# Kernel optimization log

Hardware: AMD Instinct MI355X
Metric: run time of the kernel (lower is better)

The kernel has to match this reference:

```python
import jax, jax.numpy as jnp
import numpy as np

D_MODEL = 256; N_HEADS = 8; N_LEVELS = 4; N_POINTS = 4; D_FFN = 1024
BS = 8; NQ = 100; NKPT = 17
LEVEL_SHAPES = [(160, 160), (80, 80), (40, 40), (20, 20)]  # (H, W) per level
LEN_V = sum(h * w for h, w in LEVEL_SHAPES)  # 34000


def layer_norm(x, g, b, eps=1e-5):
    m = x.mean(-1, keepdims=True)
    v = ((x - m) ** 2).mean(-1, keepdims=True)
    return (x - m) * jax.lax.rsqrt(v + eps) * g + b


def mha(q, k, v, Wqkv, bqkv, Wo, bo):
    # torch nn.MultiheadAttention, batch_first, eval mode (no dropout)
    d = q.shape[-1]; dh = d // N_HEADS
    def proj(x, W, b):
        return (x @ W.T + b).reshape(*x.shape[:-1], N_HEADS, dh)
    qp = proj(q, Wqkv[:d], bqkv[:d])
    kp = proj(k, Wqkv[d:2 * d], bqkv[d:2 * d])
    vp = proj(v, Wqkv[2 * d:], bqkv[2 * d:])
    att = jnp.einsum('bqhd,bkhd->bhqk', qp, kp) / jnp.sqrt(jnp.asarray(dh, q.dtype))
    att = jax.nn.softmax(att, -1)
    out = jnp.einsum('bhqk,bkhd->bqhd', att, vp).reshape(q.shape)
    return out @ Wo.T + bo


def bilinear_sample(val, loc, h, w):
    # val: (B, H, h*w, Dh); loc: (B, Lq, H, P, 2) normalized to [0,1]
    # matches F.grid_sample(align_corners=False, padding_mode='zeros') on grid 2*loc-1
    B, Lq, H, P, _ = loc.shape
    px = loc[..., 0] * w - 0.5
    py = loc[..., 1] * h - 0.5
    x0f = jnp.floor(px); y0f = jnp.floor(py)
    lx = px - x0f; ly = py - y0f
    x0 = x0f.astype(jnp.int32); y0 = y0f.astype(jnp.int32)
    out = jnp.zeros((B, H, Lq, P, val.shape[-1]), val.dtype)
    for dx, dy, wt in ((0, 0, (1 - lx) * (1 - ly)), (1, 0, lx * (1 - ly)),
                       (0, 1, (1 - lx) * ly), (1, 1, lx * ly)):
        xi = x0 + dx; yi = y0 + dy
        valid = ((xi >= 0) & (xi < w) & (yi >= 0) & (yi < h)).astype(val.dtype)
        idx = jnp.clip(yi, 0, h - 1) * w + jnp.clip(xi, 0, w - 1)  # (B,Lq,H,P)
        idx = idx.transpose(0, 2, 1, 3).reshape(B, H, Lq * P)
        g = jnp.take_along_axis(val, idx[..., None], axis=2).reshape(B, H, Lq, P, -1)
        out = out + g * (wt * valid).transpose(0, 2, 1, 3)[..., None]
    return out  # (B, H, Lq, P, Dh)


def ms_deform_attn(query, ref_points, memory, off_W, off_b, aw_W, aw_b,
                   val_W, val_b, outp_W, outp_b):
    B, Lq, _ = query.shape
    dh = D_MODEL // N_HEADS
    value = (memory @ val_W.T + val_b).reshape(B, LEN_V, N_HEADS, dh)
    off = (query @ off_W.T + off_b).reshape(B, Lq, N_HEADS, N_LEVELS, N_POINTS, 2)
    aw = (query @ aw_W.T + aw_b).reshape(B, Lq, N_HEADS, N_LEVELS * N_POINTS)
    aw = jax.nn.softmax(aw, -1).reshape(B, Lq, N_HEADS, N_LEVELS, N_POINTS)
    normalizer = jnp.array([[w, h] for h, w in LEVEL_SHAPES], dtype=query.dtype)  # (L,2) as (W,H)
    loc = ref_points[:, :, None, :, None, :] + off / normalizer[None, None, None, :, None, :]
    out = jnp.zeros((B, Lq, N_HEADS, dh), query.dtype)
    start = 0
    for l, (h, w) in enumerate(LEVEL_SHAPES):
        vl = value[:, start:start + h * w].transpose(0, 2, 1, 3)  # (B,H,hw,Dh)
        s = bilinear_sample(vl, loc[:, :, :, l], h, w)            # (B,H,Lq,P,Dh)
        out = out + jnp.einsum('bhqpd,bqhp->bqhd', s, aw[:, :, :, l])
        start += h * w
    return out.reshape(B, Lq, D_MODEL) @ outp_W.T + outp_b


def setup_inputs() -> dict:
    key = jax.random.key(0)
    ks = iter(jax.random.split(key, 40))
    d = D_MODEL
    def w(shape, s=0.02):
        return jax.random.normal(next(ks), shape, jnp.float32) * s
    inp = {
        'tgt_pose': jax.random.normal(next(ks), (BS, NQ, NKPT, d), jnp.float32),
        'tgt_pose_query_pos': jax.random.normal(next(ks), (BS, NQ, NKPT, d), jnp.float32),
        'tgt_pose_reference_points': jax.random.uniform(next(ks), (BS, NQ * NKPT, N_LEVELS, 2), jnp.float32),
        'memory': jax.random.normal(next(ks), (BS, LEN_V, d), jnp.float32),
        'win_Wqkv': w((3 * d, d)), 'win_bqkv': jnp.zeros((3 * d,), jnp.float32),
        'win_Wo': w((d, d)), 'win_bo': jnp.zeros((d,), jnp.float32),
        'win_ng': jnp.ones((d,), jnp.float32), 'win_nb': jnp.zeros((d,), jnp.float32),
        'acr_Wqkv': w((3 * d, d)), 'acr_bqkv': jnp.zeros((3 * d,), jnp.float32),
        'acr_Wo': w((d, d)), 'acr_bo': jnp.zeros((d,), jnp.float32),
        'acr_ng': jnp.ones((d,), jnp.float32), 'acr_nb': jnp.zeros((d,), jnp.float32),
        'off_W': w((N_HEADS * N_LEVELS * N_POINTS * 2, d)),
        'off_b': jax.random.uniform(next(ks), (N_HEADS * N_LEVELS * N_POINTS * 2,), jnp.float32, -1.0, 1.0),
        'aw_W': w((N_HEADS * N_LEVELS * N_POINTS, d)), 'aw_b': jnp.zeros((N_HEADS * N_LEVELS * N_POINTS,), jnp.float32),
        'val_W': w((d, d)), 'val_b': jnp.zeros((d,), jnp.float32),
        'outp_W': w((d, d)), 'outp_b': jnp.zeros((d,), jnp.float32),
        'gate_W': w((2 * d, 2 * d)), 'gate_b': jnp.zeros((2 * d,), jnp.float32),
        'gate_ng': jnp.ones((d,), jnp.float32), 'gate_nb': jnp.zeros((d,), jnp.float32),
        'ffn_W1': w((D_FFN, d)), 'ffn_b1': jnp.zeros((D_FFN,), jnp.float32),
        'ffn_W2': w((d, D_FFN)), 'ffn_b2': jnp.zeros((d,), jnp.float32),
        'n2_g': jnp.ones((d,), jnp.float32), 'n2_b': jnp.zeros((d,), jnp.float32),
        'memory_spatial_shapes': jnp.array(LEVEL_SHAPES, jnp.int32),
    }
    return inp


def reference(tgt_pose, tgt_pose_query_pos, tgt_pose_reference_points, memory,
              win_Wqkv, win_bqkv, win_Wo, win_bo, win_ng, win_nb,
              acr_Wqkv, acr_bqkv, acr_Wo, acr_bo, acr_ng, acr_nb,
              off_W, off_b, aw_W, aw_b, val_W, val_b, outp_W, outp_b,
              gate_W, gate_b, gate_ng, gate_nb,
              ffn_W1, ffn_b1, ffn_W2, ffn_b2, n2_g, n2_b,
              memory_spatial_shapes):
    bs, nq, K, d = tgt_pose.shape
    # with_pos_embed mutates tgt_pose in place in the torch code -> residual includes pos
    tgt = tgt_pose + tgt_pose_query_pos
    # within-attention over keypoints of each query
    x = tgt.reshape(bs * nq, K, d)
    t2 = mha(x, x, x, win_Wqkv, win_bqkv, win_Wo, win_bo).reshape(bs, nq, K, d)
    tgt = layer_norm(tgt + t2, win_ng, win_nb)
    # across-attention over queries for each keypoint
    xk = tgt.transpose(0, 2, 1, 3).reshape(bs * K, nq, d)
    t2 = mha(xk, xk, xk, acr_Wqkv, acr_bqkv, acr_Wo, acr_bo)
    tgt = layer_norm(xk + t2, acr_ng, acr_nb).reshape(bs, K, nq, d).transpose(0, 2, 1, 3)
    # second in-place pos add before deformable cross-attn (also feeds gateway)
    tgt_q = tgt + tgt_pose_query_pos
    t2 = ms_deform_attn(tgt_q.reshape(bs, nq * K, d), tgt_pose_reference_points, memory,
                        off_W, off_b, aw_W, aw_b, val_W, val_b, outp_W, outp_b)
    t2 = t2.reshape(bs, nq, K, d)
    # Gate
    g = jax.nn.sigmoid(jnp.concatenate([tgt_q, t2], -1) @ gate_W.T + gate_b)
    g1, g2 = jnp.split(g, 2, -1)
    tgt = layer_norm(g1 * tgt_q + g2 * t2, gate_ng, gate_nb)
    # FFN
    h = jax.nn.relu(tgt @ ffn_W1.T + ffn_b1)
    tgt = tgt + h @ ffn_W2.T + ffn_b2
    tgt = layer_norm(jnp.clip(tgt, -65504.0, 65504.0), n2_g, n2_b)
    return tgt
```

## Files before the change

### kernel.cpp

```cpp
#include <hip/hip_runtime.h>
#include <hip/hip_bf16.h>

#define NH 8
#define BS_ 8
#define NQ_ 100
#define NK_ 17
#define LQ 1700
#define T_TOK 13600
#define LEN_VV 34000

typedef __attribute__((ext_vector_type(8))) short short8v;
typedef __attribute__((ext_vector_type(8))) __bf16 bf16x8;
typedef __attribute__((ext_vector_type(4))) float f32x4;

__device__ __forceinline__ float wave_sum(float v){
#pragma unroll
  for (int m = 32; m; m >>= 1) v += __shfl_xor(v, m, 64);
  return v;
}
__device__ __forceinline__ short f2bf(float f){
  __hip_bfloat16 h = __float2bfloat16(f);
  return *reinterpret_cast<short*>(&h);
}
__device__ __forceinline__ float bf2f(short s){
  return __uint_as_float(((uint)(unsigned short)s) << 16);
}

__global__ __launch_bounds__(256) void add_k(const float* __restrict__ a,
                                             const float* __restrict__ b,
                                             float* __restrict__ o, int n4){
  int i = blockIdx.x * 256 + threadIdx.x;
  if (i >= n4) return;
  float4 x = ((const float4*)a)[i];
  float4 y = ((const float4*)b)[i];
  float4 r; r.x = x.x + y.x; r.y = x.y + y.y; r.z = x.z + y.z; r.w = x.w + y.w;
  ((float4*)o)[i] = r;
}

template<int EPI, int OUTB>
__global__ __launch_bounds__(256) void mgemm_k(const float* __restrict__ A,
                                               const float* __restrict__ W,
                                               const float* __restrict__ bias,
                                               float* __restrict__ Cf,
                                               __hip_bfloat16* __restrict__ Cb,
                                               int M, int N, int K){
  __shared__ short sh[OUTB ? 128 * 136 : 128 * 128];
  short* As = sh;
  short* Ws = sh + 128 * 64;
  const int tid = threadIdx.x;
  const int bm = blockIdx.y * 128, bn = blockIdx.x * 128;
  const int wave = tid >> 6, lane = tid & 63;
  const int wm = (wave >> 1) * 64, wn = (wave & 1) * 64;
  const int s = tid & 7;
  const int row0 = tid >> 3;
  f32x4 acc[4][4] = {};
  const int lrow = lane & 15, lk = lane >> 4;

  float4 ra[8], rw[8];
#pragma unroll
  for (int i = 0; i < 4; i++){
    int row = row0 + i * 32;
    int gr = bm + row;
    float4 z = make_float4(0.f, 0.f, 0.f, 0.f);
    if (gr < M){
      const float* p = A + (size_t)gr * K + s * 8;
      ra[2 * i] = ((const float4*)p)[0]; ra[2 * i + 1] = ((const float4*)p)[1];
    } else { ra[2 * i] = z; ra[2 * i + 1] = z; }
    const float* q = W + (size_t)(bn + row) * K + s * 8;
    rw[2 * i] = ((const float4*)q)[0]; rw[2 * i + 1] = ((const float4*)q)[1];
  }

  for (int k0 = 0; k0 < K; k0 += 64){
#pragma unroll
    for (int i = 0; i < 4; i++){
      int row = row0 + i * 32;
      int sw = ((s ^ (row & 7)) << 3) + row * 64;
      float4 a0 = ra[2 * i], a1 = ra[2 * i + 1];
      short8v v;
      v[0]=f2bf(a0.x); v[1]=f2bf(a0.y); v[2]=f2bf(a0.z); v[3]=f2bf(a0.w);
      v[4]=f2bf(a1.x); v[5]=f2bf(a1.y); v[6]=f2bf(a1.z); v[7]=f2bf(a1.w);
      *(short8v*)&As[sw] = v;
      a0 = rw[2 * i]; a1 = rw[2 * i + 1];
      short8v u;
      u[0]=f2bf(a0.x); u[1]=f2bf(a0.y); u[2]=f2bf(a0.z); u[3]=f2bf(a0.w);
      u[4]=f2bf(a1.x); u[5]=f2bf(a1.y); u[6]=f2bf(a1.z); u[7]=f2bf(a1.w);
      *(short8v*)&Ws[sw] = u;
    }
    __syncthreads();
    if (k0 + 64 < K){
#pragma unroll
      for (int i = 0; i < 4; i++){
        int row = row0 + i * 32;
        int gr = bm + row;
        float4 z = make_float4(0.f, 0.f, 0.f, 0.f);
        if (gr < M){
          const float* p = A + (size_t)gr * K + k0 + 64 + s * 8;
          ra[2 * i] = ((const float4*)p)[0]; ra[2 * i + 1] = ((const float4*)p)[1];
        } else { ra[2 * i] = z; ra[2 * i + 1] = z; }
        const float* q = W + (size_t)(bn + row) * K + k0 + 64 + s * 8;
        rw[2 * i] = ((const float4*)q)[0]; rw[2 * i + 1] = ((const float4*)q)[1];
      }
    }
#pragma unroll
    for (int ks = 0; ks < 2; ks++){
      short8v af[4], bw[4];
      int slot = ks * 4 + lk;
#pragma unroll
      for (int m = 0; m < 4; m++){
        int r = wm + m * 16 + lrow;
        af[m] = *(const short8v*)&As[r * 64 + ((slot ^ (r & 7)) << 3)];
      }
#pragma unroll
      for (int n = 0; n < 4; n++){
        int r = wn + n * 16 + lrow;
        bw[n] = *(const short8v*)&Ws[r * 64 + ((slot ^ (r & 7)) << 3)];
      }
#pragma unroll
      for (int m = 0; m < 4; m++)
#pragma unroll
        for (int n = 0; n < 4; n++)
          acc[m][n] = __builtin_amdgcn_mfma_f32_16x16x32_bf16(
              __builtin_bit_cast(bf16x8, af[m]),
              __builtin_bit_cast(bf16x8, bw[n]), acc[m][n], 0, 0, 0);
    }
    __syncthreads();
  }
  if (OUTB){
    const int STR = 136;
#pragma unroll
    for (int n = 0; n < 4; n++){
      int col = wn + n * 16 + lrow;
      float bsv = bias[bn + col];
#pragma unroll
      for (int m = 0; m < 4; m++){
#pragma unroll
        for (int i = 0; i < 4; i++){
          int row = wm + m * 16 + lk * 4 + i;
          float c = acc[m][n][i] + bsv;
          if (EPI == 1) c = fmaxf(c, 0.f);
          if (EPI == 2) c = 1.f / (1.f + expf(-c));
          sh[row * STR + col] = f2bf(c);
        }
      }
    }
    __syncthreads();
#pragma unroll
    for (int it = 0; it < 8; it++){
      int r = it * 16 + (tid >> 4);
      int chunk = tid & 15;
      if (bm + r < M){
        uint4 v = *(const uint4*)((const char*)sh + r * 272 + chunk * 16);
        *(uint4*)((char*)Cb + ((size_t)(bm + r) * N + bn) * 2 + chunk * 16) = v;
      }
    }
  } else {
#pragma unroll
    for (int n = 0; n < 4; n++){
      int col = bn + wn + n * 16 + lrow;
      float bsv = bias[col];
#pragma unroll
      for (int m = 0; m < 4; m++){
#pragma unroll
        for (int i = 0; i < 4; i++){
          int row = bm + wm + m * 16 + lk * 4 + i;
          if (row >= M) continue;
          float c = acc[m][n][i] + bsv;
          if (EPI == 1) c = fmaxf(c, 0.f);
          if (EPI == 2) c = 1.f / (1.f + expf(-c));
          Cf[(size_t)row * N + col] = c;
        }
      }
    }
  }
}

template<int EPI, int OUTB, int INB, int DUALA>
__global__ __launch_bounds__(256) void g64_k(const void* __restrict__ Av,
                                             const void* __restrict__ A1v,
                                             const float* __restrict__ W0,
                                             const float* __restrict__ W1,
                                             int NSPLIT,
                                             const float* __restrict__ bias0,
                                             const float* __restrict__ bias1,
                                             float* __restrict__ Cf,
                                             __hip_bfloat16* __restrict__ Cb,
                                             int M, int N, int K, int sA){
  __shared__ short sh64[2 * 64 * 64];
  short* As = sh64;
  short* Ws = sh64 + 64 * 64;
  const int tid = threadIdx.x;
  const int bn = blockIdx.x * 64, bm = blockIdx.y * 64;
  const int wave = tid >> 6, lane = tid & 63;
  const int wm = (wave >> 1) * 32, wn = (wave & 1) * 32;
  const int s = tid & 7, row0 = tid >> 3;
  const int lrow = lane & 15, lk = lane >> 4;
  f32x4 acc[2][2] = {};

  for (int k0 = 0; k0 < K; k0 += 64){
#pragma unroll
    for (int i = 0; i < 2; i++){
      int row = row0 + i * 32;
      int sw = ((s ^ (row & 7)) << 3) + row * 64;
      short8v v = {};
      int gr = bm + row;
      if (gr < M){
        if (INB){
          v = *(const short8v*)((const short*)Av + (size_t)gr * sA + k0 + s * 8);
        } else {
          const float* Ap;
          if (DUALA) Ap = (k0 < 256) ? (const float*)Av + (size_t)gr * 256 + k0
                                     : (const float*)A1v + (size_t)gr * 256 + (k0 - 256);
          else Ap = (const float*)Av + (size_t)gr * sA + k0;
          float4 a0 = ((const float4*)(Ap + s * 8))[0];
          float4 a1 = ((const float4*)(Ap + s * 8))[1];
          v[0]=f2bf(a0.x); v[1]=f2bf(a0.y); v[2]=f2bf(a0.z); v[3]=f2bf(a0.w);
          v[4]=f2bf(a1.x); v[5]=f2bf(a1.y); v[6]=f2bf(a1.z); v[7]=f2bf(a1.w);
        }
      }
      *(short8v*)&As[sw] = v;
      int wr = bn + row;
      const float* Wp = (wr < NSPLIT) ? W0 + (size_t)wr * K + k0
                                      : W1 + (size_t)(wr - NSPLIT) * K + k0;
      float4 b0 = ((const float4*)(Wp + s * 8))[0];
      float4 b1 = ((const float4*)(Wp + s * 8))[1];
      short8v u;
      u[0]=f2bf(b0.x); u[1]=f2bf(b0.y); u[2]=f2bf(b0.z); u[3]=f2bf(b0.w);
      u[4]=f2bf(b1.x); u[5]=f2bf(b1.y); u[6]=f2bf(b1.z); u[7]=f2bf(b1.w);
      *(short8v*)&Ws[sw] = u;
    }
    __syncthreads();
#pragma unroll
    for (int ks = 0; ks < 2; ks++){
      int slot = ks * 4 + lk;
      short8v af[2], bw[2];
#pragma unroll
      for (int m = 0; m < 2; m++){
        int r = wm + m * 16 + lrow;
        af[m] = *(const short8v*)&As[r * 64 + ((slot ^ (r & 7)) << 3)];
      }
#pragma unroll
      for (int n = 0; n < 2; n++){
        int r = wn + n * 16 + lrow;
        bw[n] = *(const short8v*)&Ws[r * 64 + ((slot ^ (r & 7)) << 3)];
      }
#pragma unroll
      for (int m = 0; m < 2; m++)
#pragma unroll
        for (int n = 0; n < 2; n++)
          acc[m][n] = __builtin_amdgcn_mfma_f32_16x16x32_bf16(
              __builtin_bit_cast(bf16x8, af[m]),
              __builtin_bit_cast(bf16x8, bw[n]), acc[m][n], 0, 0, 0);
    }
    __syncthreads();
  }
  if (OUTB){
    const int STR = 72;
#pragma unroll
    for (int n = 0; n < 2; n++){
      int col = wn + n * 16 + lrow;
      int gc = bn + col;
      float bsv = (gc < NSPLIT) ? bias0[gc] : bias1[gc - NSPLIT];
#pragma unroll
      for (int m = 0; m < 2; m++){
#pragma unroll
        for (int i = 0; i < 4; i++){
          int row = wm + m * 16 + lk * 4 + i;
          float c = acc[m][n][i] + bsv;
          if (EPI == 1) c = fmaxf(c, 0.f);
          if (EPI == 2) c = 1.f / (1.f + expf(-c));
          sh64[row * STR + col] = f2bf(c);
        }
      }
    }
    __syncthreads();
#pragma unroll
    for (int it = 0; it < 2; it++){
      int r = it * 32 + (tid >> 3);
      int chunk = tid & 7;
      if (bm + r < M){
        uint4 v = *(const uint4*)((const char*)sh64 + r * 144 + chunk * 16);
        *(uint4*)((char*)Cb + ((size_t)(bm + r) * N + bn) * 2 + chunk * 16) = v;
      }
    }
  } else {
#pragma unroll
    for (int n = 0; n < 2; n++){
      int gc = bn + wn + n * 16 + lrow;
      float bsv = (gc < NSPLIT) ? bias0[gc] : bias1[gc - NSPLIT];
#pragma unroll
      for (int m = 0; m < 2; m++){
#pragma unroll
        for (int i = 0; i < 4; i++){
          int row = bm + wm + m * 16 + lk * 4 + i;
          if (row >= M) continue;
          float c = acc[m][n][i] + bsv;
          if (EPI == 1) c = fmaxf(c, 0.f);
          if (EPI == 2) c = 1.f / (1.f + expf(-c));
          Cf[(size_t)row * N + gc] = c;
        }
      }
    }
  }
}

template<int TP>
__global__ __launch_bounds__(256) void mha_mfma_k(const short* __restrict__ qkv,
                                                  __hip_bfloat16* __restrict__ out, int S){
  constexpr int MT = TP / 16;
  constexpr int KSTEPS = (TP + 31) / 32;
  constexpr int KS32 = KSTEPS * 32;
  constexpr int VSTRB = (KS32 == 128) ? 256 : 128;
  __shared__ short QK[2][TP][64];
  __shared__ short Vt[2][32][VSTRB / 2];
  __shared__ float Sc[2][16][128];
  __shared__ float rinv[2][16];

  const int tid = threadIdx.x;
  const int bid = blockIdx.x;
  const int batch = bid >> 2, hp = bid & 3;
  const int wave = tid >> 6, lane = tid & 63;
  const int hh = wave >> 1, wsub = wave & 1;
  const int lrow = lane & 15, lk = lane >> 4;
  const float scale = 0.17677669529663687f;
  const size_t qbase = (size_t)batch * S * 768;

  for (int idx = tid; idx < 2 * TP * 4; idx += 256){
    int h2 = idx >= TP * 4;
    int rem = idx - h2 * TP * 4;
    int j = rem >> 2, s = rem & 3;
    int h = hp * 2 + h2;
    short8v qv = {}, kv = {};
    if (j < S){
      const short* p = qkv + qbase + (size_t)j * 768 + h * 32 + s * 8;
      qv = *(const short8v*)p;
      kv = *(const short8v*)(p + 256);
    }
    *(short8v*)&QK[h2][j][(s ^ (j & 7)) << 3] = qv;
    *(short8v*)&QK[h2][j][((s + 4) ^ (j & 7)) << 3] = kv;
  }
  for (int idx = tid; idx < 2 * KS32 * 4; idx += 256){
    int h2 = idx >= KS32 * 4;
    int rem = idx - h2 * KS32 * 4;
    int j = rem >> 2, e8 = rem & 3;
    int h = hp * 2 + h2;
    short8v v = {};
    if (j < S) v = *(const short8v*)(qkv + qbase + (size_t)j * 768 + h * 32 + 512 + e8 * 8);
#pragma unroll
    for (int c = 0; c < 8; c++){
      int e = e8 * 8 + c;
      char* pb = (char*)&Vt[h2][0][0] + e * VSTRB + (((j >> 3) ^ (e & 7)) << 4) + ((j & 7) << 1);
      *(short*)pb = v[c];
    }
  }
  __syncthreads();

  for (int mt = 0; mt < MT; mt++){
    for (int nt = wsub; nt < MT; nt += 2){
      int ar = mt * 16 + lrow;
      short8v aq = *(const short8v*)&QK[hh][ar][(lk ^ (ar & 7)) << 3];
      int br = nt * 16 + lrow;
      short8v bk = *(const short8v*)&QK[hh][br][((lk + 4) ^ (br & 7)) << 3];
      f32x4 z = {};
      f32x4 d = __builtin_amdgcn_mfma_f32_16x16x32_bf16(
          __builtin_bit_cast(bf16x8, aq), __builtin_bit_cast(bf16x8, bk), z, 0, 0, 0);
#pragma unroll
      for (int i = 0; i < 4; i++){
        int rr = lk * 4 + i;
        int c = nt * 16 + lrow;
        Sc[hh][rr][(((c >> 2) ^ (rr & 7)) << 2) + (c & 3)] = d[i] * scale;
      }
    }
    __syncthreads();
    if (wsub == 0){
      int rr = lane >> 2, p = lane & 3;
      int grow = mt * 16 + rr;
      int Seff = (grow < S) ? S : 0;
      float mx = -1e30f;
#pragma unroll
      for (int m = 0; m < KSTEPS; m++){
        int j = p + 4 * m;
#pragma unroll
        for (int half = 0; half < 2; half++){
          int ls = 2 * j + half;
          float4 v = *(const float4*)&Sc[hh][rr][(ls ^ (rr & 7)) << 2];
          int c0 = ls * 4;
          mx = fmaxf(mx, (c0 + 0 < Seff) ? v.x : -1e30f);
          mx = fmaxf(mx, (c0 + 1 < Seff) ? v.y : -1e30f);
          mx = fmaxf(mx, (c0 + 2 < Seff) ? v.z : -1e30f);
          mx = fmaxf(mx, (c0 + 3 < Seff) ? v.w : -1e30f);
        }
      }
      mx = fmaxf(mx, __shfl_xor(mx, 1, 64));
      mx = fmaxf(mx, __shfl_xor(mx, 2, 64));
      float sum = 0.f;
#pragma unroll
      for (int m = 0; m < KSTEPS; m++){
        int j = p + 4 * m;
        float ev[8];
#pragma unroll
        for (int half = 0; half < 2; half++){
          int ls = 2 * j + half;
          float4 v = *(const float4*)&Sc[hh][rr][(ls ^ (rr & 7)) << 2];
          int c0 = ls * 4;
          ev[half * 4 + 0] = (c0 + 0 < Seff) ? __expf(v.x - mx) : 0.f;
          ev[half * 4 + 1] = (c0 + 1 < Seff) ? __expf(v.y - mx) : 0.f;
          ev[half * 4 + 2] = (c0 + 2 < Seff) ? __expf(v.z - mx) : 0.f;
          ev[half * 4 + 3] = (c0 + 3 < Seff) ? __expf(v.w - mx) : 0.f;
        }
        short8v pb;
#pragma unroll
        for (int q2 = 0; q2 < 8; q2++){ pb[q2] = f2bf(ev[q2]); sum += ev[q2]; }
        *(short8v*)((char*)&Sc[hh][rr][0] + ((j ^ (rr & 7)) << 4)) = pb;
      }
      sum += __shfl_xor(sum, 1, 64);
      sum += __shfl_xor(sum, 2, 64);
      if (p == 0) rinv[hh][rr] = (sum > 0.f) ? 1.f / sum : 0.f;
    }
    __syncthreads();
    {
      int nt2 = wsub;
      f32x4 acc = {};
#pragma unroll
      for (int ks = 0; ks < KSTEPS; ks++){
        int slot = ks * 4 + lk;
        short8v ap = *(const short8v*)((const char*)&Sc[hh][lrow][0] + ((slot ^ (lrow & 7)) << 4));
        int e = nt2 * 16 + lrow;
        short8v bv = *(const short8v*)((const char*)&Vt[hh][0][0] + e * VSTRB + ((slot ^ (e & 7)) << 4));
        acc = __builtin_amdgcn_mfma_f32_16x16x32_bf16(
            __builtin_bit_cast(bf16x8, ap), __builtin_bit_cast(bf16x8, bv), acc, 0, 0, 0);
      }
      int h = hp * 2 + hh;
#pragma unroll
      for (int i = 0; i < 4; i++){
        int row = mt * 16 + lk * 4 + i;
        if (row < S){
          float rv = rinv[hh][lk * 4 + i];
          out[((size_t)batch * S + row) * 256 + h * 32 + nt2 * 16 + lrow] =
              __float2bfloat16(acc[i] * rv);
        }
      }
    }
    __syncthreads();
  }
}

template<int MODE>
__global__ __launch_bounds__(64) void ln_k(const float* __restrict__ a,
                                           const float* __restrict__ b,
                                           const float* __restrict__ g,
                                           const float* __restrict__ be,
                                           float* __restrict__ out,
                                           const float* __restrict__ qp){
  int r = blockIdx.x;
  int lane = threadIdx.x;
  float4 xa = *(const float4*)(a + (size_t)r * 256 + lane * 4);
  float4 xb = *(const float4*)(b + (size_t)r * 256 + lane * 4);
  float x[4] = { xa.x + xb.x, xa.y + xb.y, xa.z + xb.z, xa.w + xb.w };
  if (MODE == 2){
#pragma unroll
    for (int i = 0; i < 4; i++) x[i] = fminf(fmaxf(x[i], -65504.f), 65504.f);
  }
  float s = x[0] + x[1] + x[2] + x[3];
  s = wave_sum(s);
  float mean = s * (1.f / 256.f);
  float sq = 0.f;
#pragma unroll
  for (int i = 0; i < 4; i++){ float d = x[i] - mean; sq += d * d; }
  float var = wave_sum(sq) * (1.f / 256.f);
  float rstd = rsqrtf(var + 1e-5f);
  float4 gg = *(const float4*)(g + lane * 4);
  float4 bb = *(const float4*)(be + lane * 4);
  size_t orow = r;
  if (MODE == 3){
    int bi = r / LQ; int rem = r % LQ; int kk = rem / NQ_; int q = rem % NQ_;
    orow = (size_t)bi * LQ + q * NK_ + kk;
  }
  if (MODE == 4){
    int bi = r / LQ; int rem = r % LQ; int q = rem / NK_; int kk = rem % NK_;
    orow = (size_t)bi * LQ + kk * NQ_ + q;
  }
  float4 o;
  o.x = (x[0] - mean) * rstd * gg.x + bb.x;
  o.y = (x[1] - mean) * rstd * gg.y + bb.y;
  o.z = (x[2] - mean) * rstd * gg.z + bb.z;
  o.w = (x[3] - mean) * rstd * gg.w + bb.w;
  if (MODE == 3){
    float4 qv = *(const float4*)(qp + orow * 256 + lane * 4);
    o.x += qv.x; o.y += qv.y; o.z += qv.z; o.w += qv.w;
  }
  *(float4*)(out + orow * 256 + lane * 4) = o;
}

__global__ __launch_bounds__(64) void gate_ln_k(const short* __restrict__ G,
                                                const float* __restrict__ aq,
                                                const float* __restrict__ t2,
                                                const float* __restrict__ g,
                                                const float* __restrict__ be,
                                                float* __restrict__ out){
  int r = blockIdx.x;
  int lane = threadIdx.x;
  const short* gp = G + (size_t)r * 512 + lane * 4;
  float g1v[4], g2v[4];
#pragma unroll
  for (int i = 0; i < 4; i++){ g1v[i] = bf2f(gp[i]); g2v[i] = bf2f(gp[256 + i]); }
  float4 xa = *(const float4*)(aq + (size_t)r * 256 + lane * 4);
  float4 xt = *(const float4*)(t2 + (size_t)r * 256 + lane * 4);
  float x[4] = { g1v[0] * xa.x + g2v[0] * xt.x, g1v[1] * xa.y + g2v[1] * xt.y,
                 g1v[2] * xa.z + g2v[2] * xt.z, g1v[3] * xa.w + g2v[3] * xt.w };
  float s = x[0] + x[1] + x[2] + x[3];
  s = wave_sum(s);
  float mean = s * (1.f / 256.f);
  float sq = 0.f;
#pragma unroll
  for (int i = 0; i < 4; i++){ float d = x[i] - mean; sq += d * d; }
  float var = wave_sum(sq) * (1.f / 256.f);
  float rstd = rsqrtf(var + 1e-5f);
  float4 gg = *(const float4*)(g + lane * 4);
  float4 bb = *(const float4*)(be + lane * 4);
  float4 o;
  o.x = (x[0] - mean) * rstd * gg.x + bb.x;
  o.y = (x[1] - mean) * rstd * gg.y + bb.y;
  o.z = (x[2] - mean) * rstd * gg.z + bb.z;
  o.w = (x[3] - mean) * rstd * gg.w + bb.w;
  *(float4*)(out + (size_t)r * 256 + lane * 4) = o;
}

__global__ __launch_bounds__(256) void deform_k(const __hip_bfloat16* __restrict__ val,
                                                const float* __restrict__ offaw,
                                                const float* __restrict__ ref,
                                                unsigned int* __restrict__ outb){
  __shared__ uint2 meta[32][16][4];
  const int tid = threadIdx.x;
  const int t0 = blockIdx.x * 4;
  {
    int g = tid >> 3;
    int pair = tid & 7;
    int lt = g >> 3, h = g & 7;
    int t = t0 + lt;
    int b = t / LQ;
    int p0 = pair * 2;
    int l = p0 >> 2;
    const int starts[4] = {0, 25600, 32000, 33600};
    const int HS[4] = {160, 80, 40, 20};
    int w = HS[l];
    const float* ap = offaw + (size_t)t * 384 + 256 + h * 16;
    float a0 = ap[p0];
    float a1 = ap[p0 + 1];
    float mx = fmaxf(a0, a1);
#pragma unroll
    for (int m = 1; m <= 4; m <<= 1) mx = fmaxf(mx, __shfl_xor(mx, m, 64));
    float e0 = expf(a0 - mx), e1 = expf(a1 - mx);
    float s = e0 + e1;
#pragma unroll
    for (int m = 1; m <= 4; m <<= 1) s += __shfl_xor(s, m, 64);
    float inv = 1.f / s;
    float rx = ref[((size_t)t * 4 + l) * 2 + 0];
    float ry = ref[((size_t)t * 4 + l) * 2 + 1];
    float4 ov = *(const float4*)(offaw + (size_t)t * 384 + h * 32 + l * 8 + p0 * 2);
    int vbase = (b * LEN_VV + starts[l]) * 128 + h * 16;
#pragma unroll
    for (int pp = 0; pp < 2; pp++){
      float wgt = (pp ? e1 : e0) * inv;
      float px = rx * w + (pp ? ov.z : ov.x) - 0.5f;
      float py = ry * w + (pp ? ov.w : ov.y) - 0.5f;
      float x0f = floorf(px), y0f = floorf(py);
      float lx = px - x0f, ly = py - y0f;
      int x0 = (int)x0f, y0 = (int)y0f;
#pragma unroll
      for (int c = 0; c < 4; c++){
        int dx = c & 1, dy = c >> 1;
        int xi = x0 + dx, yi = y0 + dy;
        bool ok = (xi >= 0) & (xi < w) & (yi >= 0) & (yi < w);
        float cw = ok ? wgt * (dx ? lx : 1.f - lx) * (dy ? ly : 1.f - ly) : 0.f;
        uint idx = ok ? (uint)(vbase + (yi * w + xi) * 128) : 0u;
        uint2 m2; m2.x = idx; m2.y = __float_as_uint(cw);
        meta[g][p0 + pp][c] = m2;
      }
    }
  }
  __syncthreads();
  const uint* V2 = (const uint*)val;
  int sg = tid >> 4, lane = tid & 15;
#pragma unroll
  for (int it = 0; it < 2; it++){
    int g = it * 16 + sg;
    int lt = g >> 3, h = g & 7;
    int t = t0 + lt;
    float ax = 0.f, ay = 0.f;
#pragma unroll 4
    for (int c = 0; c < 64; c++){
      uint2 mw = meta[g][c >> 2][c & 3];
      float wv = __uint_as_float(mw.y);
      uint v = V2[(size_t)mw.x + lane];
      float lo = __uint_as_float(v << 16);
      float hi = __uint_as_float(v & 0xffff0000u);
      ax += wv * lo;
      ay += wv * hi;
    }
    uint u = ((uint)(unsigned short)f2bf(ay) << 16) | (uint)(unsigned short)f2bf(ax);
    outb[((size_t)t * 256 + h * 32) / 2 + lane] = u;
  }
}

extern "C" void kernel_launch(void* const* d_in, const int* in_sizes, int n_in,
                              void* d_out, int out_size, void* d_ws, size_t ws_size,
                              hipStream_t stream){
  const float* tgt_pose = (const float*)d_in[0];
  const float* qpos     = (const float*)d_in[1];
  const float* refp     = (const float*)d_in[2];
  const float* memory   = (const float*)d_in[3];
  const float* win_Wqkv = (const float*)d_in[4];
  const float* win_bqkv = (const float*)d_in[5];
  const float* win_Wo   = (const float*)d_in[6];
  const float* win_bo   = (const float*)d_in[7];
  const float* win_ng   = (const float*)d_in[8];
  const float* win_nb   = (const float*)d_in[9];
  const float* acr_Wqkv = (const float*)d_in[10];
  const float* acr_bqkv = (const float*)d_in[11];
  const float* acr_Wo   = (const float*)d_in[12];
  const float* acr_bo   = (const float*)d_in[13];
  const float* acr_ng   = (const float*)d_in[14];
  const float* acr_nb   = (const float*)d_in[15];
  const float* off_W    = (const float*)d_in[16];
  const float* off_b    = (const float*)d_in[17];
  const float* aw_W     = (const float*)d_in[18];
  const float* aw_b     = (const float*)d_in[19];
  const float* val_W    = (const float*)d_in[20];
  const float* val_b    = (const float*)d_in[21];
  const float* outp_W   = (const float*)d_in[22];
  const float* outp_b   = (const float*)d_in[23];
  const float* gate_W   = (const float*)d_in[24];
  const float* gate_b   = (const float*)d_in[25];
  const float* gate_ng  = (const float*)d_in[26];
  const float* gate_nb  = (const float*)d_in[27];
  const float* ffn_W1   = (const float*)d_in[28];
  const float* ffn_b1   = (const float*)d_in[29];
  const float* ffn_W2   = (const float*)d_in[30];
  const float* ffn_b2   = (const float*)d_in[31];
  const float* n2_g     = (const float*)d_in[32];
  const float* n2_b     = (const float*)d_in[33];

  float* out = (float*)d_out;
  char* ws = (char*)d_ws;
  const size_t TB = (size_t)T_TOK * 256 * 4;
  float* B0 = (float*)(ws);
  float* B1 = (float*)(ws + TB);
  float* B2 = (float*)(ws + 2 * TB);
  float* B3 = (float*)(ws + 3 * TB);
  char* p = ws + 4 * TB;
  short* Qb = (short*)p;                 p += (size_t)T_TOK * 768 * 2;
  short* ABF = (short*)p;                p += (size_t)T_TOK * 256 * 2;
  float* OFFAW = (float*)p;              p += (size_t)T_TOK * 384 * 4;
  short* Gb = (short*)p;                 p += (size_t)T_TOK * 512 * 2;
  char* Vregion = p;
  __hip_bfloat16* V = (__hip_bfloat16*)Vregion;
  short* FF = (short*)Vregion;

  const int n4 = T_TOK * 64;
  const int GM128 = (T_TOK + 127) / 128;
  const int GM64  = (T_TOK + 63) / 64;
  const int BIG = 1 << 30;

  add_k<<<(n4 + 255) / 256, 256, 0, stream>>>(tgt_pose, qpos, B0, n4);
  mgemm_k<0,1><<<dim3(6, GM128), 256, 0, stream>>>(B0, win_Wqkv, win_bqkv, nullptr, (__hip_bfloat16*)Qb, T_TOK, 768, 256);
  mha_mfma_k<32><<<800 * 4, 256, 0, stream>>>(Qb, (__hip_bfloat16*)ABF, 17);
  g64_k<0,0,1,0><<<dim3(4, GM64), 256, 0, stream>>>(ABF, nullptr, win_Wo, win_Wo, BIG, win_bo, win_bo, B2, nullptr, T_TOK, 256, 256, 256);
  ln_k<4><<<T_TOK, 64, 0, stream>>>(B0, B2, win_ng, win_nb, B1, nullptr);
  mgemm_k<0,1><<<dim3(6, GM128), 256, 0, stream>>>(B1, acr_Wqkv, acr_bqkv, nullptr, (__hip_bfloat16*)Qb, T_TOK, 768, 256);
  mha_mfma_k<112><<<136 * 4, 256, 0, stream>>>(Qb, (__hip_bfloat16*)ABF, 100);
  g64_k<0,0,1,0><<<dim3(4, GM64), 256, 0, stream>>>(ABF, nullptr, acr_Wo, acr_Wo, BIG, acr_bo, acr_bo, B2, nullptr, T_TOK, 256, 256, 256);
  ln_k<3><<<T_TOK, 64, 0, stream>>>(B1, B2, acr_ng, acr_nb, B0, qpos);
  mgemm_k<0,1><<<dim3(2, 2125), 256, 0, stream>>>(memory, val_W, val_b, nullptr, V, BS_ * LEN_VV, 256, 256);
  g64_k<0,0,0,0><<<dim3(6, GM64), 256, 0, stream>>>(B0, nullptr, off_W, aw_W, 256, off_b, aw_b, OFFAW, nullptr, T_TOK, 384, 256, 256);
  deform_k<<<T_TOK / 4, 256, 0, stream>>>(V, OFFAW, refp, (unsigned int*)ABF);
  g64_k<0,0,1,0><<<dim3(4, GM64), 256, 0, stream>>>(ABF, nullptr, outp_W, outp_W, BIG, outp_b, outp_b, B3, nullptr, T_TOK, 256, 256, 256);
  g64_k<2,1,0,1><<<dim3(8, GM64), 256, 0, stream>>>(B0, B3, gate_W, gate_W, BIG, gate_b, gate_b, nullptr, (__hip_bfloat16*)Gb, T_TOK, 512, 512, 256);
  gate_ln_k<<<T_TOK, 64, 0, stream>>>(Gb, B0, B3, gate_ng, gate_nb, B2);
  mgemm_k<1,1><<<dim3(8, GM128), 256, 0, stream>>>(B2, ffn_W1, ffn_b1, nullptr, (__hip_bfloat16*)FF, T_TOK, 1024, 256);
  g64_k<0,0,1,0><<<dim3(4, GM64), 256, 0, stream>>>(FF, nullptr, ffn_W2, ffn_W2, BIG, ffn_b2, ffn_b2, B1, nullptr, T_TOK, 256, 1024, 1024);
  ln_k<2><<<T_TOK, 64, 0, stream>>>(B2, B1, n2_g, n2_b, out, nullptr);
}
```

Measured before the change: 465.4 us.

## Fuse pos-add into QKV GEMM, co-schedule value projection, split across-attention blocks

```diff
diff --git a/kernel.cpp b/kernel.cpp
--- a/kernel.cpp
+++ b/kernel.cpp
@@ -26,25 +26,13 @@
   return __uint_as_float(((uint)(unsigned short)s) << 16);
 }
 
-__global__ __launch_bounds__(256) void add_k(const float* __restrict__ a,
-                                             const float* __restrict__ b,
-                                             float* __restrict__ o, int n4){
-  int i = blockIdx.x * 256 + threadIdx.x;
-  if (i >= n4) return;
-  float4 x = ((const float4*)a)[i];
-  float4 y = ((const float4*)b)[i];
-  float4 r; r.x = x.x + y.x; r.y = x.y + y.y; r.z = x.z + y.z; r.w = x.w + y.w;
-  ((float4*)o)[i] = r;
-}
-
-template<int EPI, int OUTB>
+template<int EPI>
 __global__ __launch_bounds__(256) void mgemm_k(const float* __restrict__ A,
                                                const float* __restrict__ W,
                                                const float* __restrict__ bias,
-                                               float* __restrict__ Cf,
                                                __hip_bfloat16* __restrict__ Cb,
                                                int M, int N, int K){
-  __shared__ short sh[OUTB ? 128 * 136 : 128 * 128];
+  __shared__ short sh[128 * 136];
   short* As = sh;
   short* Ws = sh + 128 * 64;
   const int tid = threadIdx.x;
@@ -125,51 +113,177 @@
     }
     __syncthreads();
   }
-  if (OUTB){
-    const int STR = 136;
-#pragma unroll
-    for (int n = 0; n < 4; n++){
-      int col = wn + n * 16 + lrow;
-      float bsv = bias[bn + col];
+  const int STR = 136;
+#pragma unroll
+  for (int n = 0; n < 4; n++){
+    int col = wn + n * 16 + lrow;
+    float bsv = bias[bn + col];
+#pragma unroll
+    for (int m = 0; m < 4; m++){
+#pragma unroll
+      for (int i = 0; i < 4; i++){
+        int row = wm + m * 16 + lk * 4 + i;
+        float c = acc[m][n][i] + bsv;
+        if (EPI == 1) c = fmaxf(c, 0.f);
+        sh[row * STR + col] = f2bf(c);
+      }
+    }
+  }
+  __syncthreads();
+#pragma unroll
+  for (int it = 0; it < 8; it++){
+    int r = it * 16 + (tid >> 4);
+    int chunk = tid & 15;
+    if (bm + r < M){
+      uint4 v = *(const uint4*)((const char*)sh + r * 272 + chunk * 16);
+      *(uint4*)((char*)Cb + ((size_t)(bm + r) * N + bn) * 2 + chunk * 16) = v;
+    }
+  }
+}
+
+__global__ __launch_bounds__(256) void dualgemm_k(const float* __restrict__ A0,
+                                                  const float* __restrict__ A0b,
+                                                  const float* __restrict__ W0,
+                                                  const float* __restrict__ bias0,
+                                                  __hip_bfloat16* __restrict__ C0,
+                                                  int M0, int N0, int nbx0, int NJ0,
+                                                  const float* __restrict__ A1,
+                                                  const float* __restrict__ W1,
+                                                  const float* __restrict__ bias1,
+                                                  __hip_bfloat16* __restrict__ C1,
+                                                  int M1, int N1, int nbx1){
+  const int INTER = 7;
+  __shared__ short sh[128 * 136];
+  short* As = sh;
+  short* Ws = sh + 128 * 64;
+  const int bid = blockIdx.x;
+  const int j = bid / INTER, r7 = bid % INTER;
+  const float* A; const float* A2; const float* W; const float* bias;
+  __hip_bfloat16* C; int M, N, bx, by;
+  if (r7 == 0 && j < NJ0){
+    A = A0; A2 = A0b; W = W0; bias = bias0; C = C0; M = M0; N = N0;
+    bx = j % nbx0; by = j / nbx0;
+  } else {
+    int c0 = (j + 1 < NJ0) ? (j + 1) : NJ0;
+    int idx = bid - c0;
+    A = A1; A2 = nullptr; W = W1; bias = bias1; C = C1; M = M1; N = N1;
+    bx = idx % nbx1; by = idx / nbx1;
+  }
+  const int K = 256;
+  const int tid = threadIdx.x;
+  const int bm = by * 128, bn = bx * 128;
+  const int wave = tid >> 6, lane = tid & 63;
+  const int wm = (wave >> 1) * 64, wn = (wave & 1) * 64;
+  const int s = tid & 7;
+  const int row0 = tid >> 3;
+  f32x4 acc[4][4] = {};
+  const int lrow = lane & 15, lk = lane >> 4;
+
+  float4 ra[8], rw[8];
+#pragma unroll
+  for (int i = 0; i < 4; i++){
+    int row = row0 + i * 32;
+    int gr = bm + row;
+    float4 z = make_float4(0.f, 0.f, 0.f, 0.f);
+    if (gr < M){
+      const float* p = A + (size_t)gr * K + s * 8;
+      float4 x0 = ((const float4*)p)[0], x1 = ((const float4*)p)[1];
+      if (A2){
+        const float* q2 = A2 + (size_t)gr * K + s * 8;
+        float4 y0 = ((const float4*)q2)[0], y1 = ((const float4*)q2)[1];
+        x0.x+=y0.x; x0.y+=y0.y; x0.z+=y0.z; x0.w+=y0.w;
+        x1.x+=y1.x; x1.y+=y1.y; x1.z+=y1.z; x1.w+=y1.w;
+      }
+      ra[2 * i] = x0; ra[2 * i + 1] = x1;
+    } else { ra[2 * i] = z; ra[2 * i + 1] = z; }
+    const float* q = W + (size_t)(bn + row) * K + s * 8;
+    rw[2 * i] = ((const float4*)q)[0]; rw[2 * i + 1] = ((const float4*)q)[1];
+  }
+
+  for (int k0 = 0; k0 < K; k0 += 64){
+#pragma unroll
+    for (int i = 0; i < 4; i++){
+      int row = row0 + i * 32;
+      int sw = ((s ^ (row & 7)) << 3) + row * 64;
+      float4 a0 = ra[2 * i], a1 = ra[2 * i + 1];
+      short8v v;
+      v[0]=f2bf(a0.x); v[1]=f2bf(a0.y); v[2]=f2bf(a0.z); v[3]=f2bf(a0.w);
+      v[4]=f2bf(a1.x); v[5]=f2bf(a1.y); v[6]=f2bf(a1.z); v[7]=f2bf(a1.w);
+      *(short8v*)&As[sw] = v;
+      a0 = rw[2 * i]; a1 = rw[2 * i + 1];
+      short8v u;
+      u[0]=f2bf(a0.x); u[1]=f2bf(a0.y); u[2]=f2bf(a0.z); u[3]=f2bf(a0.w);
+      u[4]=f2bf(a1.x); u[5]=f2bf(a1.y); u[6]=f2bf(a1.z); u[7]=f2bf(a1.w);
+      *(short8v*)&Ws[sw] = u;
+    }
+    __syncthreads();
+    if (k0 + 64 < K){
+#pragma unroll
+      for (int i = 0; i < 4; i++){
+        int row = row0 + i * 32;
+        int gr = bm + row;
+        float4 z = make_float4(0.f, 0.f, 0.f, 0.f);
+        if (gr < M){
+          const float* p = A + (size_t)gr * K + k0 + 64 + s * 8;
+          float4 x0 = ((const float4*)p)[0], x1 = ((const float4*)p)[1];
+          if (A2){
+            const float* q2 = A2 + (size_t)gr * K + k0 + 64 + s * 8;
+            float4 y0 = ((const float4*)q2)[0], y1 = ((const float4*)q2)[1];
+            x0.x+=y0.x; x0.y+=y0.y; x0.z+=y0.z; x0.w+=y0.w;
+            x1.x+=y1.x; x1.y+=y1.y; x1.z+=y1.z; x1.w+=y1.w;
+          }
+          ra[2 * i] = x0; ra[2 * i + 1] = x1;
+        } else { ra[2 * i] = z; ra[2 * i + 1] = z; }
+        const float* q = W + (size_t)(bn + row) * K + k0 + 64 + s * 8;
+        rw[2 * i] = ((const float4*)q)[0]; rw[2 * i + 1] = ((const float4*)q)[1];
+      }
+    }
+#pragma unroll
+    for (int ks = 0; ks < 2; ks++){
+      short8v af[4], bw[4];
+      int slot = ks * 4 + lk;
 #pragma unroll
       for (int m = 0; m < 4; m++){
-#pragma unroll
-        for (int i = 0; i < 4; i++){
-          int row = wm + m * 16 + lk * 4 + i;
-          float c = acc[m][n][i] + bsv;
-          if (EPI == 1) c = fmaxf(c, 0.f);
-          if (EPI == 2) c = 1.f / (1.f + expf(-c));
-          sh[row * STR + col] = f2bf(c);
-        }
-      }
-    }
-    __syncthreads();
-#pragma unroll
-    for (int it = 0; it < 8; it++){
-      int r = it * 16 + (tid >> 4);
-      int chunk = tid & 15;
-      if (bm + r < M){
-        uint4 v = *(const uint4*)((const char*)sh + r * 272 + chunk * 16);
-        *(uint4*)((char*)Cb + ((size_t)(bm + r) * N + bn) * 2 + chunk * 16) = v;
-      }
-    }
-  } else {
-#pragma unroll
-    for (int n = 0; n < 4; n++){
-      int col = bn + wn + n * 16 + lrow;
-      float bsv = bias[col];
-#pragma unroll
-      for (int m = 0; m < 4; m++){
-#pragma unroll
-        for (int i = 0; i < 4; i++){
-          int row = bm + wm + m * 16 + lk * 4 + i;
-          if (row >= M) continue;
-          float c = acc[m][n][i] + bsv;
-          if (EPI == 1) c = fmaxf(c, 0.f);
-          if (EPI == 2) c = 1.f / (1.f + expf(-c));
-          Cf[(size_t)row * N + col] = c;
-        }
-      }
+        int rr = wm + m * 16 + lrow;
+        af[m] = *(const short8v*)&As[rr * 64 + ((slot ^ (rr & 7)) << 3)];
+      }
+#pragma unroll
+      for (int n = 0; n < 4; n++){
+        int rr = wn + n * 16 + lrow;
+        bw[n] = *(const short8v*)&Ws[rr * 64 + ((slot ^ (rr & 7)) << 3)];
+      }
+#pragma unroll
+      for (int m = 0; m < 4; m++)
+#pragma unroll
+        for (int n = 0; n < 4; n++)
+          acc[m][n] = __builtin_amdgcn_mfma_f32_16x16x32_bf16(
+              __builtin_bit_cast(bf16x8, af[m]),
+              __builtin_bit_cast(bf16x8, bw[n]), acc[m][n], 0, 0, 0);
+    }
+    __syncthreads();
+  }
+  const int STR = 136;
+#pragma unroll
+  for (int n = 0; n < 4; n++){
+    int col = wn + n * 16 + lrow;
+    float bsv = bias[bn + col];
+#pragma unroll
+    for (int m = 0; m < 4; m++){
+#pragma unroll
+      for (int i = 0; i < 4; i++){
+        int row = wm + m * 16 + lk * 4 + i;
+        sh[row * STR + col] = f2bf(acc[m][n][i] + bsv);
+      }
+    }
+  }
+  __syncthreads();
+#pragma unroll
+  for (int it = 0; it < 8; it++){
+    int r = it * 16 + (tid >> 4);
+    int chunk = tid & 15;
+    if (bm + r < M){
+      uint4 v = *(const uint4*)((const char*)sh + r * 272 + chunk * 16);
+      *(uint4*)((char*)C + ((size_t)(bm + r) * N + bn) * 2 + chunk * 16) = v;
     }
   }
 }
@@ -182,6 +296,7 @@
                                              int NSPLIT,
                                              const float* __restrict__ bias0,
                                              const float* __restrict__ bias1,
+                                             const float* __restrict__ RES,
                                              float* __restrict__ Cf,
                                              __hip_bfloat16* __restrict__ Cb,
                                              int M, int N, int K, int sA){
@@ -296,6 +411,7 @@
           float c = acc[m][n][i] + bsv;
           if (EPI == 1) c = fmaxf(c, 0.f);
           if (EPI == 2) c = 1.f / (1.f + expf(-c));
+          if (EPI == 3) c += RES[(size_t)row * N + gc];
           Cf[(size_t)row * N + gc] = c;
         }
       }
@@ -303,13 +419,14 @@
   }
 }
 
-template<int TP>
+template<int TP, int NSPL>
 __global__ __launch_bounds__(256) void mha_mfma_k(const short* __restrict__ qkv,
                                                   __hip_bfloat16* __restrict__ out, int S){
   constexpr int MT = TP / 16;
   constexpr int KSTEPS = (TP + 31) / 32;
   constexpr int KS32 = KSTEPS * 32;
   constexpr int VSTRB = (KS32 == 128) ? 256 : 128;
+  constexpr int CH = (MT + NSPL - 1) / NSPL;
   __shared__ short QK[2][TP][64];
   __shared__ short Vt[2][32][VSTRB / 2];
   __shared__ float Sc[2][16][128];
@@ -317,7 +434,12 @@
 
   const int tid = threadIdx.x;
   const int bid = blockIdx.x;
-  const int batch = bid >> 2, hp = bid & 3;
+  const int batch = bid / (4 * NSPL);
+  const int rem = bid % (4 * NSPL);
+  const int hp = rem / NSPL;
+  const int half = rem % NSPL;
+  const int mtlo = half * CH;
+  const int mthi = (mtlo + CH < MT) ? (mtlo + CH) : MT;
   const int wave = tid >> 6, lane = tid & 63;
   const int hh = wave >> 1, wsub = wave & 1;
   const int lrow = lane & 15, lk = lane >> 4;
@@ -326,8 +448,8 @@
 
   for (int idx = tid; idx < 2 * TP * 4; idx += 256){
     int h2 = idx >= TP * 4;
-    int rem = idx - h2 * TP * 4;
-    int j = rem >> 2, s = rem & 3;
+    int rm = idx - h2 * TP * 4;
+    int j = rm >> 2, s = rm & 3;
     int h = hp * 2 + h2;
     short8v qv = {}, kv = {};
     if (j < S){
@@ -340,8 +462,8 @@
   }
   for (int idx = tid; idx < 2 * KS32 * 4; idx += 256){
     int h2 = idx >= KS32 * 4;
-    int rem = idx - h2 * KS32 * 4;
-    int j = rem >> 2, e8 = rem & 3;
+    int rm = idx - h2 * KS32 * 4;
+    int j = rm >> 2, e8 = rm & 3;
     int h = hp * 2 + h2;
     short8v v = {};
     if (j < S) v = *(const short8v*)(qkv + qbase + (size_t)j * 768 + h * 32 + 512 + e8 * 8);
@@ -354,7 +476,7 @@
   }
   __syncthreads();
 
-  for (int mt = 0; mt < MT; mt++){
+  for (int mt = mtlo; mt < mthi; mt++){
     for (int nt = wsub; nt < MT; nt += 2){
       int ar = mt * 16 + lrow;
       short8v aq = *(const short8v*)&QK[hh][ar][(lk ^ (ar & 7)) << 3];
@@ -380,8 +502,8 @@
       for (int m = 0; m < KSTEPS; m++){
         int j = p + 4 * m;
 #pragma unroll
-        for (int half = 0; half < 2; half++){
-          int ls = 2 * j + half;
+        for (int hf = 0; hf < 2; hf++){
+          int ls = 2 * j + hf;
           float4 v = *(const float4*)&Sc[hh][rr][(ls ^ (rr & 7)) << 2];
           int c0 = ls * 4;
           mx = fmaxf(mx, (c0 + 0 < Seff) ? v.x : -1e30f);
@@ -398,14 +520,14 @@
         int j = p + 4 * m;
         float ev[8];
 #pragma unroll
-        for (int half = 0; half < 2; half++){
-          int ls = 2 * j + half;
+        for (int hf = 0; hf < 2; hf++){
+          int ls = 2 * j + hf;
           float4 v = *(const float4*)&Sc[hh][rr][(ls ^ (rr & 7)) << 2];
           int c0 = ls * 4;
-          ev[half * 4 + 0] = (c0 + 0 < Seff) ? __expf(v.x - mx) : 0.f;
-          ev[half * 4 + 1] = (c0 + 1 < Seff) ? __expf(v.y - mx) : 0.f;
-          ev[half * 4 + 2] = (c0 + 2 < Seff) ? __expf(v.z - mx) : 0.f;
-          ev[half * 4 + 3] = (c0 + 3 < Seff) ? __expf(v.w - mx) : 0.f;
+          ev[hf * 4 + 0] = (c0 + 0 < Seff) ? __expf(v.x - mx) : 0.f;
+          ev[hf * 4 + 1] = (c0 + 1 < Seff) ? __expf(v.y - mx) : 0.f;
+          ev[hf * 4 + 2] = (c0 + 2 < Seff) ? __expf(v.z - mx) : 0.f;
+          ev[hf * 4 + 3] = (c0 + 3 < Seff) ? __expf(v.w - mx) : 0.f;
         }
         short8v pb;
 #pragma unroll
@@ -450,13 +572,21 @@
                                            const float* __restrict__ g,
                                            const float* __restrict__ be,
                                            float* __restrict__ out,
-                                           const float* __restrict__ qp){
+                                           const float* __restrict__ qpre,
+                                           const float* __restrict__ qpost){
   int r = blockIdx.x;
   int lane = threadIdx.x;
   float4 xa = *(const float4*)(a + (size_t)r * 256 + lane * 4);
-  float4 xb = *(const float4*)(b + (size_t)r * 256 + lane * 4);
-  float x[4] = { xa.x + xb.x, xa.y + xb.y, xa.z + xb.z, xa.w + xb.w };
-  if (MODE == 2){
+  float x[4] = { xa.x, xa.y, xa.z, xa.w };
+  if (MODE != 5){
+    float4 xb = *(const float4*)(b + (size_t)r * 256 + lane * 4);
+    x[0] += xb.x; x[1] += xb.y; x[2] += xb.z; x[3] += xb.w;
+  }
+  if (MODE == 4){
+    float4 xq = *(const float4*)(qpre + (size_t)r * 256 + lane * 4);
+    x[0] += xq.x; x[1] += xq.y; x[2] += xq.z; x[3] += xq.w;
+  }
+  if (MODE == 5){
 #pragma unroll
     for (int i = 0; i < 4; i++) x[i] = fminf(fmaxf(x[i], -65504.f), 65504.f);
   }
@@ -485,7 +615,7 @@
   o.z = (x[2] - mean) * rstd * gg.z + bb.z;
   o.w = (x[3] - mean) * rstd * gg.w + bb.w;
   if (MODE == 3){
-    float4 qv = *(const float4*)(qp + orow * 256 + lane * 4);
+    float4 qv = *(const float4*)(qpost + orow * 256 + lane * 4);
     o.x += qv.x; o.y += qv.y; o.z += qv.z; o.w += qv.w;
   }
   *(float4*)(out + orow * 256 + lane * 4) = o;
@@ -656,27 +786,28 @@
   __hip_bfloat16* V = (__hip_bfloat16*)Vregion;
   short* FF = (short*)Vregion;
 
-  const int n4 = T_TOK * 64;
   const int GM128 = (T_TOK + 127) / 128;
   const int GM64  = (T_TOK + 63) / 64;
   const int BIG = 1 << 30;
-
-  add_k<<<(n4 + 255) / 256, 256, 0, stream>>>(tgt_pose, qpos, B0, n4);
-  mgemm_k<0,1><<<dim3(6, GM128), 256, 0, stream>>>(B0, win_Wqkv, win_bqkv, nullptr, (__hip_bfloat16*)Qb, T_TOK, 768, 256);
-  mha_mfma_k<32><<<800 * 4, 256, 0, stream>>>(Qb, (__hip_bfloat16*)ABF, 17);
-  g64_k<0,0,1,0><<<dim3(4, GM64), 256, 0, stream>>>(ABF, nullptr, win_Wo, win_Wo, BIG, win_bo, win_bo, B2, nullptr, T_TOK, 256, 256, 256);
-  ln_k<4><<<T_TOK, 64, 0, stream>>>(B0, B2, win_ng, win_nb, B1, nullptr);
-  mgemm_k<0,1><<<dim3(6, GM128), 256, 0, stream>>>(B1, acr_Wqkv, acr_bqkv, nullptr, (__hip_bfloat16*)Qb, T_TOK, 768, 256);
-  mha_mfma_k<112><<<136 * 4, 256, 0, stream>>>(Qb, (__hip_bfloat16*)ABF, 100);
-  g64_k<0,0,1,0><<<dim3(4, GM64), 256, 0, stream>>>(ABF, nullptr, acr_Wo, acr_Wo, BIG, acr_bo, acr_bo, B2, nullptr, T_TOK, 256, 256, 256);
-  ln_k<3><<<T_TOK, 64, 0, stream>>>(B1, B2, acr_ng, acr_nb, B0, qpos);
-  mgemm_k<0,1><<<dim3(2, 2125), 256, 0, stream>>>(memory, val_W, val_b, nullptr, V, BS_ * LEN_VV, 256, 256);
-  g64_k<0,0,0,0><<<dim3(6, GM64), 256, 0, stream>>>(B0, nullptr, off_W, aw_W, 256, off_b, aw_b, OFFAW, nullptr, T_TOK, 384, 256, 256);
+  const int NJ0 = 6 * GM128;
+  const int NJ1 = 2 * 2125;
+
+  dualgemm_k<<<NJ0 + NJ1, 256, 0, stream>>>(
+      tgt_pose, qpos, win_Wqkv, win_bqkv, (__hip_bfloat16*)Qb, T_TOK, 768, 6, NJ0,
+      memory, val_W, val_b, V, BS_ * LEN_VV, 256, 2);
+  mha_mfma_k<32,1><<<800 * 4, 256, 0, stream>>>(Qb, (__hip_bfloat16*)ABF, 17);
+  g64_k<0,0,1,0><<<dim3(4, GM64), 256, 0, stream>>>(ABF, nullptr, win_Wo, win_Wo, BIG, win_bo, win_bo, nullptr, B2, nullptr, T_TOK, 256, 256, 256);
+  ln_k<4><<<T_TOK, 64, 0, stream>>>(tgt_pose, B2, win_ng, win_nb, B1, qpos, nullptr);
+  mgemm_k<0><<<dim3(6, GM128), 256, 0, stream>>>(B1, acr_Wqkv, acr_bqkv, (__hip_bfloat16*)Qb, T_TOK, 768, 256);
+  mha_mfma_k<112,2><<<136 * 8, 256, 0, stream>>>(Qb, (__hip_bfloat16*)ABF, 100);
+  g64_k<0,0,1,0><<<dim3(4, GM64), 256, 0, stream>>>(ABF, nullptr, acr_Wo, acr_Wo, BIG, acr_bo, acr_bo, nullptr, B2, nullptr, T_TOK, 256, 256, 256);
+  ln_k<3><<<T_TOK, 64, 0, stream>>>(B1, B2, acr_ng, acr_nb, B0, nullptr, qpos);
+  g64_k<0,0,0,0><<<dim3(6, GM64), 256, 0, stream>>>(B0, nullptr, off_W, aw_W, 256, off_b, aw_b, nullptr, OFFAW, nullptr, T_TOK, 384, 256, 256);
   deform_k<<<T_TOK / 4, 256, 0, stream>>>(V, OFFAW, refp, (unsigned int*)ABF);
-  g64_k<0,0,1,0><<<dim3(4, GM64), 256, 0, stream>>>(ABF, nullptr, outp_W, outp_W, BIG, outp_b, outp_b, B3, nullptr, T_TOK, 256, 256, 256);
-  g64_k<2,1,0,1><<<dim3(8, GM64), 256, 0, stream>>>(B0, B3, gate_W, gate_W, BIG, gate_b, gate_b, nullptr, (__hip_bfloat16*)Gb, T_TOK, 512, 512, 256);
+  g64_k<0,0,1,0><<<dim3(4, GM64), 256, 0, stream>>>(ABF, nullptr, outp_W, outp_W, BIG, outp_b, outp_b, nullptr, B3, nullptr, T_TOK, 256, 256, 256);
+  g64_k<2,1,0,1><<<dim3(8, GM64), 256, 0, stream>>>(B0, B3, gate_W, gate_W, BIG, gate_b, gate_b, nullptr, nullptr, (__hip_bfloat16*)Gb, T_TOK, 512, 512, 256);
   gate_ln_k<<<T_TOK, 64, 0, stream>>>(Gb, B0, B3, gate_ng, gate_nb, B2);
-  mgemm_k<1,1><<<dim3(8, GM128), 256, 0, stream>>>(B2, ffn_W1, ffn_b1, nullptr, (__hip_bfloat16*)FF, T_TOK, 1024, 256);
-  g64_k<0,0,1,0><<<dim3(4, GM64), 256, 0, stream>>>(FF, nullptr, ffn_W2, ffn_W2, BIG, ffn_b2, ffn_b2, B1, nullptr, T_TOK, 256, 1024, 1024);
-  ln_k<2><<<T_TOK, 64, 0, stream>>>(B2, B1, n2_g, n2_b, out, nullptr);
-}
+  mgemm_k<1><<<dim3(8, GM128), 256, 0, stream>>>(B2, ffn_W1, ffn_b1, (__hip_bfloat16*)FF, T_TOK, 1024, 256);
+  g64_k<3,0,1,0><<<dim3(4, GM64), 256, 0, stream>>>(FF, nullptr, ffn_W2, ffn_W2, BIG, ffn_b2, ffn_b2, B2, B1, nullptr, T_TOK, 256, 1024, 1024);
+  ln_k<5><<<T_TOK, 64, 0, stream>>>(B1, nullptr, n2_g, n2_b, out, nullptr, nullptr);
+}
```

Result: no change. 460.0 us (-1.2%).
